# Kernel tuning notes

Measured on AMD Instinct MI355X. Metric: run time of the kernel, lower is better.

The kernel has to match this reference:

```python
import jax, jax.numpy as jnp
import numpy as np

B, N, M = 8, 8192, 2048
C1, C2 = 128, 256
H = 256  # mlp hidden/out channels


def setup_inputs() -> dict:
    key = jax.random.key(0)
    ks = jax.random.split(key, 8)
    return {
        "unknown": jax.random.normal(ks[0], (B, N, 3), dtype=jnp.float32),
        "known": jax.random.normal(ks[1], (B, M, 3), dtype=jnp.float32),
        "unknow_feats": jax.random.normal(ks[2], (B, C1, N), dtype=jnp.float32),
        "known_feats": jax.random.normal(ks[3], (B, C2, M), dtype=jnp.float32),
        "W1": jax.random.normal(ks[4], (H, C1 + C2), dtype=jnp.float32) * 0.02,
        "b1": jnp.zeros((H,), dtype=jnp.float32),
        "W2": jax.random.normal(ks[5], (H, H), dtype=jnp.float32) * 0.02,
        "b2": jnp.zeros((H,), dtype=jnp.float32),
    }


def _three_nn(unknown, known):
    # squared pairwise distances (B, n, m)
    d2 = jnp.sum((unknown[:, :, None, :] - known[:, None, :, :]) ** 2, axis=-1)
    neg_d2_top, idx = jax.lax.top_k(-d2, 3)  # 3 smallest distances
    dist = jnp.sqrt(jnp.maximum(-neg_d2_top, 0.0))  # (B, n, 3)
    return dist, idx


def _three_interpolate(features, idx, weight):
    # features: (B, c, m); idx, weight: (B, n, 3) -> (B, c, n)
    Bc, c, m = features.shape
    n = idx.shape[1]
    idx_flat = jnp.broadcast_to(idx.reshape(Bc, 1, n * 3), (Bc, c, n * 3))
    gathered = jnp.take_along_axis(features, idx_flat, axis=2).reshape(Bc, c, n, 3)
    return jnp.sum(gathered * weight[:, None, :, :], axis=-1)


def reference(unknown, known, unknow_feats, known_feats, W1, b1, W2, b2):
    dist, idx = _three_nn(unknown, known)
    dist_recip = 1.0 / (dist + 1e-8)
    weight = dist_recip / jnp.sum(dist_recip, axis=2, keepdims=True)  # (B, n, 3)
    interpolated = _three_interpolate(known_feats, idx, weight)  # (B, C2, n)
    new_features = jnp.concatenate([interpolated, unknow_feats], axis=1)  # (B, C1+C2, n)
    # shared MLP: two conv1x1 (bias, no BN) + ReLU
    h = jax.nn.relu(jnp.einsum('oc,bcn->bon', W1, new_features) + b1[None, :, None])
    out = jax.nn.relu(jnp.einsum('oc,bcn->bon', W2, h) + b2[None, :, None])
    return out
```

## Files before the change

### kernel.cpp

```cpp
#include <hip/hip_runtime.h>

using bf16x8 = __attribute__((ext_vector_type(8))) short;
using f32x4  = __attribute__((ext_vector_type(4))) float;

constexpr int Bb = 8, Nn = 8192, Mm = 2048, C1 = 128, C2 = 256, Hh = 256, K1 = 384;
constexpr int KT1 = K1 / 32;
constexpr int KT2 = Hh / 32;
constexpr int RT = Hh / 16;
constexpr int NQ = 4;
constexpr int MQ = Mm / NQ;

constexpr int TR_BLOCKS = 4096;
constexpr int WP_BLOCKS = (KT1 * RT * 64 + KT2 * RT * 64) / 256;
constexpr int NN_BASE   = TR_BLOCKS + WP_BLOCKS;
constexpr int NN_BLOCKS = Bb * 32 * NQ;

__device__ __forceinline__ short f2bf(float x) {
  union { float f; unsigned u; } v; v.f = x;
  unsigned r = v.u + 0x7fff + ((v.u >> 16) & 1);
  return (short)(r >> 16);
}

__device__ __forceinline__ void merge3(float a0, float a1, float a2, int A0, int A1, int A2,
                                       float b0, float b1, float b2, int B0, int B1, int B2,
                                       float& m0, float& m1, float& m2,
                                       int& j0, int& j1, int& j2) {
  bool ta = a0 <= b0;
  m0 = ta ? a0 : b0; j0 = ta ? A0 : B0;
  float na0 = ta ? a1 : a0, na1 = ta ? a2 : a1;
  int   nA0 = ta ? A1 : A0, nA1 = ta ? A2 : A1;
  float nb0 = ta ? b0 : b1, nb1 = ta ? b1 : b2;
  int   nB0 = ta ? B0 : B1, nB1 = ta ? B1 : B2;
  ta = na0 <= nb0;
  m1 = ta ? na0 : nb0; j1 = ta ? nA0 : nB0;
  float ma0 = ta ? na1 : na0; int mA0 = ta ? nA1 : nA0;
  float mb0 = ta ? nb0 : nb1; int mB0 = ta ? nB0 : nB1;
  ta = ma0 <= mb0;
  m2 = ta ? ma0 : mb0; j2 = ta ? mA0 : mB0;
}

__global__ __launch_bounds__(256) void prep_nn_k(const float* __restrict__ kf,
                                                 float* __restrict__ kfT,
                                                 const float* __restrict__ W1,
                                                 const float* __restrict__ W2,
                                                 short* __restrict__ W1f,
                                                 short* __restrict__ W2f,
                                                 const float* __restrict__ unknown,
                                                 const float* __restrict__ known,
                                                 float* __restrict__ pd,
                                                 int* __restrict__ pi) {
  __shared__ float tile[32][33];
  int bid = blockIdx.x, tid = threadIdx.x;

  if (bid < TR_BLOCKS) {
    int cx = bid & 63, ry = (bid >> 6) & 7, z = bid >> 9;
    const int R = C2, C = Mm;
    const float* src = kf + (size_t)z * R * C;
    float* dst = kfT + (size_t)z * R * C;
    int c0 = cx * 32, r0 = ry * 32;
    int tx = tid & 31, ty = tid >> 5;
#pragma unroll
    for (int rr = ty; rr < 32; rr += 8) tile[rr][tx] = src[(size_t)(r0 + rr) * C + c0 + tx];
    __syncthreads();
#pragma unroll
    for (int cc = ty; cc < 32; cc += 8) dst[(size_t)(c0 + cc) * R + r0 + tx] = tile[tx][cc];
    return;
  }

  if (bid < NN_BASE) {
    int id = (bid - TR_BLOCKS) * 256 + tid;
    const int n1 = KT1 * RT * 64;
    const int n2 = KT2 * RT * 64;
    if (id < n1) {
      int lane = id & 63, t = id >> 6;
      int kt = t / RT, rt = t % RT;
      int m = rt * 16 + (lane & 15), k0 = kt * 32 + (lane >> 4) * 8;
      bf16x8 f;
#pragma unroll
      for (int j = 0; j < 8; ++j) f[j] = f2bf(W1[(size_t)m * K1 + k0 + j]);
      *(bf16x8*)(W1f + (size_t)id * 8) = f;
    } else if (id < n1 + n2) {
      int id2 = id - n1;
      int lane = id2 & 63, t = id2 >> 6;
      int kt = t / RT, rt = t % RT;
      int m = rt * 16 + (lane & 15), k0 = kt * 32 + (lane >> 4) * 8;
      bf16x8 f;
#pragma unroll
      for (int j = 0; j < 8; ++j) f[j] = f2bf(W2[(size_t)m * Hh + k0 + j]);
      *(bf16x8*)(W2f + (size_t)id2 * 8) = f;
    }
    return;
  }

  {
    int bidn = bid - NN_BASE;
    int b = bidn >> 7, rem = bidn & 127;
    int q = rem & 3, nblk = rem >> 2;
    int n = nblk * 256 + tid;
    const float* kb = known + ((size_t)b * Mm + q * MQ) * 3;

    size_t ui = ((size_t)b * Nn + n) * 3;
    float ux = unknown[ui], uy = unknown[ui + 1], uz = unknown[ui + 2];
    float d0 = 1e30f, d1 = 1e30f, d2 = 1e30f;
    int i0 = 0, i1 = 0, i2 = 0;
    int gbase = q * MQ;

#define NN_STEP(xx, yy, zz, qq)                                         \
  {                                                                     \
    float dx = ux - (xx), dy = uy - (yy), dz = uz - (zz);               \
    float dd = dx * dx + dy * dy + dz * dz;                             \
    if (__any(dd < d2)) {    \
      int jm = gbase + jb + (qq);                                       \
      bool c0 = dd < d0, c1 = dd < d1, c2 = dd < d2;                    \
      d2 = c1 ? d1 : (c2 ? dd : d2); i2 = c1 ? i1 : (c2 ? jm : i2);     \
      d1 = c0 ? d0 : (c1 ? dd : d1); i1 = c0 ? i0 : (c1 ? jm : i1);     \
      d0 = c0 ? dd : d0;             i0 = c0 ? jm : i0;                 \
    }                                                                   \
  }

    for (int jb = 0; jb < MQ; jb += 4) {
      int jbu = __builtin_amdgcn_readfirstlane(jb);
      const float* kq = kb + 3 * (size_t)jbu;
      float k0x = kq[0], k0y = kq[1],  k0z = kq[2];
      float k1x = kq[3], k1y = kq[4],  k1z = kq[5];
      float k2x = kq[6], k2y = kq[7],  k2z = kq[8];
      float k3x = kq[9], k3y = kq[10], k3z = kq[11];
      NN_STEP(k0x, k0y, k0z, 0)
      NN_STEP(k1x, k1y, k1z, 1)
      NN_STEP(k2x, k2y, k2z, 2)
      NN_STEP(k3x, k3y, k3z, 3)
    }
#undef NN_STEP

    size_t o = (((size_t)b * Nn + n) * NQ + q) * 3;
    pd[o] = d0; pd[o + 1] = d1; pd[o + 2] = d2;
    pi[o] = i0; pi[o + 1] = i1; pi[o + 2] = i2;
  }
}

__global__ __launch_bounds__(256) void fused_gemm_k(
    const float* __restrict__ uf, const float* __restrict__ kfT,
    const short* __restrict__ W1f, const float* __restrict__ b1,
    const short* __restrict__ W2f, const float* __restrict__ b2,
    const float* __restrict__ pd, const int* __restrict__ pi,
    float* __restrict__ out) {
  __shared__ short Fs[KT1 * 4 * 64 * 8];
  __shared__ short Hs[KT2 * 4 * 64 * 8];
  int bid = blockIdx.x;
  int b = bid >> 7, bt = bid & 127;
  int tid = threadIdx.x, lane = tid & 63, wv = tid >> 6;
  int quad = lane >> 4, col = lane & 15;

  {
    int n = bt * 64 + wv * 16 + col;
    size_t pbase = (size_t)(b * Nn + n) * (NQ * 3);
    float4 da = *(const float4*)&pd[pbase];
    float4 db = *(const float4*)&pd[pbase + 4];
    float4 dc = *(const float4*)&pd[pbase + 8];
    int4 ia = *(const int4*)&pi[pbase];
    int4 ib = *(const int4*)&pi[pbase + 4];
    int4 ic = *(const int4*)&pi[pbase + 8];
    float t0, t1, t2, u0, u1, u2, m0, m1, m2;
    int T0, T1, T2, U0, U1, U2, g0, g1, g2;
    merge3(da.x, da.y, da.z, ia.x, ia.y, ia.z,
           da.w, db.x, db.y, ia.w, ib.x, ib.y, t0, t1, t2, T0, T1, T2);
    merge3(db.z, db.w, dc.x, ib.z, ib.w, ic.x,
           dc.y, dc.z, dc.w, ic.y, ic.z, ic.w, u0, u1, u2, U0, U1, U2);
    merge3(t0, t1, t2, T0, T1, T2, u0, u1, u2, U0, U1, U2,
           m0, m1, m2, g0, g1, g2);
    float s0 = sqrtf(m0), s1 = sqrtf(m1), s2 = sqrtf(m2);
    float r0 = 1.f / (s0 + 1e-8f), r1 = 1.f / (s1 + 1e-8f), r2 = 1.f / (s2 + 1e-8f);
    float rs = 1.f / (r0 + r1 + r2);
    float w0 = r0 * rs, w1 = r1 * rs, w2 = r2 * rs;

    const float* kfb = kfT + (size_t)b * Mm * C2;
#pragma unroll 4
    for (int kt = 0; kt < 8; ++kt) {
      int c0 = kt * 32 + quad * 8;
      float4 p0a = *(const float4*)&kfb[(size_t)g0 * C2 + c0];
      float4 p0b = *(const float4*)&kfb[(size_t)g0 * C2 + c0 + 4];
      float4 p1a = *(const float4*)&kfb[(size_t)g1 * C2 + c0];
      float4 p1b = *(const float4*)&kfb[(size_t)g1 * C2 + c0 + 4];
      float4 p2a = *(const float4*)&kfb[(size_t)g2 * C2 + c0];
      float4 p2b = *(const float4*)&kfb[(size_t)g2 * C2 + c0 + 4];
      bf16x8 f;
      f[0] = f2bf(w0 * p0a.x + w1 * p1a.x + w2 * p2a.x);
      f[1] = f2bf(w0 * p0a.y + w1 * p1a.y + w2 * p2a.y);
      f[2] = f2bf(w0 * p0a.z + w1 * p1a.z + w2 * p2a.z);
      f[3] = f2bf(w0 * p0a.w + w1 * p1a.w + w2 * p2a.w);
      f[4] = f2bf(w0 * p0b.x + w1 * p1b.x + w2 * p2b.x);
      f[5] = f2bf(w0 * p0b.y + w1 * p1b.y + w2 * p2b.y);
      f[6] = f2bf(w0 * p0b.z + w1 * p1b.z + w2 * p2b.z);
      f[7] = f2bf(w0 * p0b.w + w1 * p1b.w + w2 * p2b.w);
      *(bf16x8*)&Fs[((kt * 4 + wv) * 64 + lane) * 8] = f;
    }
#pragma unroll 2
    for (int kt = 8; kt < 12; ++kt) {
      int c1 = (kt - 8) * 32 + quad * 8;
      bf16x8 f;
#pragma unroll
      for (int j = 0; j < 8; ++j)
        f[j] = f2bf(uf[((size_t)b * C1 + c1 + j) * Nn + n]);
      *(bf16x8*)&Fs[((kt * 4 + wv) * 64 + lane) * 8] = f;
    }
  }
  __syncthreads();

  f32x4 acc[4][4];
#pragma unroll
  for (int r = 0; r < 4; ++r)
#pragma unroll
    for (int c = 0; c < 4; ++c) acc[r][c] = (f32x4){0.f, 0.f, 0.f, 0.f};

  for (int kt = 0; kt < KT1; ++kt) {
    bf16x8 Afr[4], Bfr[4];
#pragma unroll
    for (int r = 0; r < 4; ++r)
      Afr[r] = *(const bf16x8*)(W1f + ((size_t)(kt * RT + wv * 4 + r) * 64 + lane) * 8);
#pragma unroll
    for (int c = 0; c < 4; ++c)
      Bfr[c] = *(const bf16x8*)&Fs[((kt * 4 + c) * 64 + lane) * 8];
#pragma unroll
    for (int r = 0; r < 4; ++r)
#pragma unroll
      for (int c = 0; c < 4; ++c)
        acc[r][c] = __builtin_amdgcn_mfma_f32_16x16x32_bf16(Afr[r], Bfr[c], acc[r][c], 0, 0, 0);
  }

#pragma unroll
  for (int r = 0; r < 4; ++r) {
    f32x4 bq = *(const f32x4*)&b1[wv * 64 + r * 16 + quad * 4];
#pragma unroll
    for (int c = 0; c < 4; ++c)
#pragma unroll
      for (int reg = 0; reg < 4; ++reg)
        acc[r][c][reg] = fmaxf(acc[r][c][reg] + bq[reg], 0.f);
  }
  {
    int addr_lo = (((quad & 1) * 2) * 16 + col) * 4;
    bool hiSel = lane >= 32;
#pragma unroll
    for (int ktl = 0; ktl < 2; ++ktl)
#pragma unroll
      for (int c = 0; c < 4; ++c) {
        bf16x8 f;
#pragma unroll
        for (int j = 0; j < 8; ++j) {
          int addr = addr_lo + (j >> 2) * 64;
          int lo = __builtin_amdgcn_ds_bpermute(addr, __float_as_int(acc[ktl * 2][c][j & 3]));
          int hi = __builtin_amdgcn_ds_bpermute(addr, __float_as_int(acc[ktl * 2 + 1][c][j & 3]));
          f[j] = f2bf(__int_as_float(hiSel ? hi : lo));
        }
        *(bf16x8*)&Hs[(((wv * 2 + ktl) * 4 + c) * 64 + lane) * 8] = f;
      }
  }
  __syncthreads();

  f32x4 acc2[4][4];
#pragma unroll
  for (int r = 0; r < 4; ++r)
#pragma unroll
    for (int c = 0; c < 4; ++c) acc2[r][c] = (f32x4){0.f, 0.f, 0.f, 0.f};

  for (int kt = 0; kt < KT2; ++kt) {
    bf16x8 Afr[4], Bfr[4];
#pragma unroll
    for (int r = 0; r < 4; ++r)
      Afr[r] = *(const bf16x8*)(W2f + ((size_t)(kt * RT + wv * 4 + r) * 64 + lane) * 8);
#pragma unroll
    for (int c = 0; c < 4; ++c)
      Bfr[c] = *(const bf16x8*)&Hs[((kt * 4 + c) * 64 + lane) * 8];
#pragma unroll
    for (int r = 0; r < 4; ++r)
#pragma unroll
      for (int c = 0; c < 4; ++c)
        acc2[r][c] = __builtin_amdgcn_mfma_f32_16x16x32_bf16(Afr[r], Bfr[c], acc2[r][c], 0, 0, 0);
  }

#pragma unroll
  for (int r = 0; r < 4; ++r) {
    f32x4 bq = *(const f32x4*)&b2[wv * 64 + r * 16 + quad * 4];
#pragma unroll
    for (int c = 0; c < 4; ++c)
#pragma unroll
      for (int reg = 0; reg < 4; ++reg) {
        int rowg = wv * 64 + r * 16 + quad * 4 + reg;
        int n = bt * 64 + c * 16 + col;
        out[((size_t)b * Hh + rowg) * Nn + n] = fmaxf(acc2[r][c][reg] + bq[reg], 0.f);
      }
  }
}

extern "C" void kernel_launch(void* const* d_in, const int* in_sizes, int n_in,
                              void* d_out, int out_size, void* d_ws, size_t ws_size,
                              hipStream_t stream) {
  const float* unknown = (const float*)d_in[0];
  const float* known   = (const float*)d_in[1];
  const float* uf      = (const float*)d_in[2];
  const float* kf      = (const float*)d_in[3];
  const float* W1      = (const float*)d_in[4];
  const float* b1      = (const float*)d_in[5];
  const float* W2      = (const float*)d_in[6];
  const float* b2      = (const float*)d_in[7];
  float* out = (float*)d_out;

  char* p = (char*)d_ws;
  float* kfT = (float*)p;  p += (size_t)Bb * Mm * C2 * 4;
  short* W1f = (short*)p;  p += (size_t)KT1 * RT * 64 * 8 * 2;
  short* W2f = (short*)p;  p += (size_t)KT2 * RT * 64 * 8 * 2;
  float* pd  = (float*)p;  p += (size_t)Bb * Nn * NQ * 3 * 4;
  int* pi    = (int*)p;    p += (size_t)Bb * Nn * NQ * 3 * 4;

  prep_nn_k<<<dim3(NN_BASE + NN_BLOCKS), dim3(256), 0, stream>>>(
      kf, kfT, W1, W2, W1f, W2f, unknown, known, pd, pi);
  fused_gemm_k<<<dim3(Bb * (Nn / 64)), dim3(256), 0, stream>>>(
      uf, kfT, W1f, b1, W2f, b2, pd, pi, out);
}
```

Measured before the change: 254.9 us.

## Stage known points in LDS as SoA, use packed bf16 convert, alias Hs onto Fs

In the nearest-neighbour phase, each block first copies its quarter of the known points into shared memory as separate x/y/z arrays. The inner loop then reads them with float4 LDS loads instead of scalar global loads. The float-to-bf16 conversions now use the hardware packed cvt_pk_bf16_f32 builtin when it is available, in place of manual rounding. The GEMM kernel also reuses the Fs shared buffer for Hs, which cuts its LDS footprint and may raise occupancy, at the cost of an extra barrier after the first MFMA loop.

```diff
diff --git a/kernel.cpp b/kernel.cpp
--- a/kernel.cpp
+++ b/kernel.cpp
@@ -19,6 +19,17 @@
   union { float f; unsigned u; } v; v.f = x;
   unsigned r = v.u + 0x7fff + ((v.u >> 16) & 1);
   return (short)(r >> 16);
+}
+
+__device__ __forceinline__ unsigned pk2bf(float a, float b) {
+#if defined(__has_builtin) && __has_builtin(__builtin_amdgcn_cvt_pk_bf16_f32)
+  typedef __attribute__((ext_vector_type(2))) __bf16 bf2_t;
+  bf2_t r = __builtin_amdgcn_cvt_pk_bf16_f32(a, b);
+  union { bf2_t v; unsigned u; } cvt; cvt.v = r;
+  return cvt.u;
+#else
+  return (unsigned)(unsigned short)f2bf(a) | ((unsigned)(unsigned short)f2bf(b) << 16);
+#endif
 }
 
 __device__ __forceinline__ void merge3(float a0, float a1, float a2, int A0, int A1, int A2,
@@ -49,10 +60,11 @@
                                                  const float* __restrict__ known,
                                                  float* __restrict__ pd,
                                                  int* __restrict__ pi) {
-  __shared__ float tile[32][33];
+  __shared__ float smem[1536];
   int bid = blockIdx.x, tid = threadIdx.x;
 
   if (bid < TR_BLOCKS) {
+    float (*tile)[33] = reinterpret_cast<float(*)[33]>(smem);
     int cx = bid & 63, ry = (bid >> 6) & 7, z = bid >> 9;
     const int R = C2, C = Mm;
     const float* src = kf + (size_t)z * R * C;
@@ -93,11 +105,18 @@
   }
 
   {
+    float* kx = smem;
+    float* ky = smem + MQ;
+    float* kz = smem + 2 * MQ;
     int bidn = bid - NN_BASE;
     int b = bidn >> 7, rem = bidn & 127;
     int q = rem & 3, nblk = rem >> 2;
     int n = nblk * 256 + tid;
     const float* kb = known + ((size_t)b * Mm + q * MQ) * 3;
+    for (int p = tid; p < MQ; p += 256) {
+      kx[p] = kb[3 * p]; ky[p] = kb[3 * p + 1]; kz[p] = kb[3 * p + 2];
+    }
+    __syncthreads();
 
     size_t ui = ((size_t)b * Nn + n) * 3;
     float ux = unknown[ui], uy = unknown[ui + 1], uz = unknown[ui + 2];
@@ -119,16 +138,13 @@
   }
 
     for (int jb = 0; jb < MQ; jb += 4) {
-      int jbu = __builtin_amdgcn_readfirstlane(jb);
-      const float* kq = kb + 3 * (size_t)jbu;
-      float k0x = kq[0], k0y = kq[1],  k0z = kq[2];
-      float k1x = kq[3], k1y = kq[4],  k1z = kq[5];
-      float k2x = kq[6], k2y = kq[7],  k2z = kq[8];
-      float k3x = kq[9], k3y = kq[10], k3z = kq[11];
-      NN_STEP(k0x, k0y, k0z, 0)
-      NN_STEP(k1x, k1y, k1z, 1)
-      NN_STEP(k2x, k2y, k2z, 2)
-      NN_STEP(k3x, k3y, k3z, 3)
+      float4 xs = *(const float4*)&kx[jb];
+      float4 ys = *(const float4*)&ky[jb];
+      float4 zs = *(const float4*)&kz[jb];
+      NN_STEP(xs.x, ys.x, zs.x, 0)
+      NN_STEP(xs.y, ys.y, zs.y, 1)
+      NN_STEP(xs.z, ys.z, zs.z, 2)
+      NN_STEP(xs.w, ys.w, zs.w, 3)
     }
 #undef NN_STEP
 
@@ -145,7 +161,7 @@
     const float* __restrict__ pd, const int* __restrict__ pi,
     float* __restrict__ out) {
   __shared__ short Fs[KT1 * 4 * 64 * 8];
-  __shared__ short Hs[KT2 * 4 * 64 * 8];
+  short* Hs = Fs;
   int bid = blockIdx.x;
   int b = bid >> 7, bt = bid & 127;
   int tid = threadIdx.x, lane = tid & 63, wv = tid >> 6;
@@ -183,25 +199,30 @@
       float4 p1b = *(const float4*)&kfb[(size_t)g1 * C2 + c0 + 4];
       float4 p2a = *(const float4*)&kfb[(size_t)g2 * C2 + c0];
       float4 p2b = *(const float4*)&kfb[(size_t)g2 * C2 + c0 + 4];
-      bf16x8 f;
-      f[0] = f2bf(w0 * p0a.x + w1 * p1a.x + w2 * p2a.x);
-      f[1] = f2bf(w0 * p0a.y + w1 * p1a.y + w2 * p2a.y);
-      f[2] = f2bf(w0 * p0a.z + w1 * p1a.z + w2 * p2a.z);
-      f[3] = f2bf(w0 * p0a.w + w1 * p1a.w + w2 * p2a.w);
-      f[4] = f2bf(w0 * p0b.x + w1 * p1b.x + w2 * p2b.x);
-      f[5] = f2bf(w0 * p0b.y + w1 * p1b.y + w2 * p2b.y);
-      f[6] = f2bf(w0 * p0b.z + w1 * p1b.z + w2 * p2b.z);
-      f[7] = f2bf(w0 * p0b.w + w1 * p1b.w + w2 * p2b.w);
-      *(bf16x8*)&Fs[((kt * 4 + wv) * 64 + lane) * 8] = f;
+      float e0 = w0 * p0a.x + w1 * p1a.x + w2 * p2a.x;
+      float e1 = w0 * p0a.y + w1 * p1a.y + w2 * p2a.y;
+      float e2 = w0 * p0a.z + w1 * p1a.z + w2 * p2a.z;
+      float e3 = w0 * p0a.w + w1 * p1a.w + w2 * p2a.w;
+      float e4 = w0 * p0b.x + w1 * p1b.x + w2 * p2b.x;
+      float e5 = w0 * p0b.y + w1 * p1b.y + w2 * p2b.y;
+      float e6 = w0 * p0b.z + w1 * p1b.z + w2 * p2b.z;
+      float e7 = w0 * p0b.w + w1 * p1b.w + w2 * p2b.w;
+      uint4 packed;
+      packed.x = pk2bf(e0, e1); packed.y = pk2bf(e2, e3);
+      packed.z = pk2bf(e4, e5); packed.w = pk2bf(e6, e7);
+      *(uint4*)&Fs[((kt * 4 + wv) * 64 + lane) * 8] = packed;
     }
 #pragma unroll 2
     for (int kt = 8; kt < 12; ++kt) {
       int c1 = (kt - 8) * 32 + quad * 8;
-      bf16x8 f;
+      float e[8];
 #pragma unroll
       for (int j = 0; j < 8; ++j)
-        f[j] = f2bf(uf[((size_t)b * C1 + c1 + j) * Nn + n]);
-      *(bf16x8*)&Fs[((kt * 4 + wv) * 64 + lane) * 8] = f;
+        e[j] = uf[((size_t)b * C1 + c1 + j) * Nn + n];
+      uint4 packed;
+      packed.x = pk2bf(e[0], e[1]); packed.y = pk2bf(e[2], e[3]);
+      packed.z = pk2bf(e[4], e[5]); packed.w = pk2bf(e[6], e[7]);
+      *(uint4*)&Fs[((kt * 4 + wv) * 64 + lane) * 8] = packed;
     }
   }
   __syncthreads();
@@ -226,6 +247,7 @@
       for (int c = 0; c < 4; ++c)
         acc[r][c] = __builtin_amdgcn_mfma_f32_16x16x32_bf16(Afr[r], Bfr[c], acc[r][c], 0, 0, 0);
   }
+  __syncthreads();
 
 #pragma unroll
   for (int r = 0; r < 4; ++r) {
@@ -243,15 +265,18 @@
     for (int ktl = 0; ktl < 2; ++ktl)
 #pragma unroll
       for (int c = 0; c < 4; ++c) {
-        bf16x8 f;
+        float e[8];
 #pragma unroll
         for (int j = 0; j < 8; ++j) {
           int addr = addr_lo + (j >> 2) * 64;
           int lo = __builtin_amdgcn_ds_bpermute(addr, __float_as_int(acc[ktl * 2][c][j & 3]));
           int hi = __builtin_amdgcn_ds_bpermute(addr, __float_as_int(acc[ktl * 2 + 1][c][j & 3]));
-          f[j] = f2bf(__int_as_float(hiSel ? hi : lo));
+          e[j] = __int_as_float(hiSel ? hi : lo);
         }
-        *(bf16x8*)&Hs[(((wv * 2 + ktl) * 4 + c) * 64 + lane) * 8] = f;
+        uint4 packed;
+        packed.x = pk2bf(e[0], e[1]); packed.y = pk2bf(e[2], e[3]);
+        packed.z = pk2bf(e[4], e[5]); packed.w = pk2bf(e[6], e[7]);
+        *(uint4*)&Hs[(((wv * 2 + ktl) * 4 + c) * 64 + lane) * 8] = packed;
       }
   }
   __syncthreads();
```

After: 257.8 us. About the same (+1.2%).
